# Performance work log

Measured on AMD Instinct MI355X. Metric: run time of the kernel, lower is better.

## Reference

```python
import jax, jax.numpy as jnp
import numpy as np

F32 = jnp.float32
FP8_MAX = 448.0          # E4M3 max normal
MIN_NORM_EXP = -6.0      # smallest normal exponent for E4M3 (bias 7)


def _floor_log2(a):
    """Exact floor(log2(a)) for a>0 (with correction for fp rounding); 0 -> 0."""
    a_safe = jnp.where(a > 0, a, 1.0)
    e = jnp.floor(jnp.log2(a_safe))
    p = jnp.exp2(e)
    e = jnp.where(a_safe >= 2.0 * p, e + 1.0, jnp.where(a_safe < p, e - 1.0, e))
    return jax.lax.stop_gradient(e)


def quant_e4m3(x):
    """Round-to-nearest-even quantization to FP8 E4M3 (saturating, no NaN)."""
    a = jnp.abs(x)
    e = jnp.maximum(_floor_log2(a), MIN_NORM_EXP)
    step = jnp.exp2(e - 3.0)                 # mantissa ULP (3 mantissa bits)
    q = jnp.round(a / step) * step           # jnp.round = round-half-even
    q = jnp.minimum(q, FP8_MAX)
    q = jnp.where(a > 0, q, 0.0)
    return jnp.where(x < 0, -q, q)


def bits_to_float(b):
    """Decode [..., 8] spike bits (sign, e3..e0, m2..m0) to float32 E4M3 value."""
    sign = 1.0 - 2.0 * b[..., 0]
    exp = b[..., 1] * 8.0 + b[..., 2] * 4.0 + b[..., 3] * 2.0 + b[..., 4]
    man = b[..., 5] * 4.0 + b[..., 6] * 2.0 + b[..., 7]
    mag = jnp.where(exp > 0,
                    (1.0 + man / 8.0) * jnp.exp2(exp - 7.0),   # normal
                    (man / 8.0) * jnp.exp2(MIN_NORM_EXP))       # subnormal
    return sign * mag


def float_to_bits(x):
    """Encode an FP8-representable float32 into [..., 8] spike bits."""
    sgn = (x < 0).astype(F32)
    a = jnp.abs(x)
    e = jnp.clip(_floor_log2(a), MIN_NORM_EXP, 8.0)
    is_norm = a >= jnp.exp2(MIN_NORM_EXP)
    ef = jnp.where(is_norm, e + 7.0, 0.0)
    man = jnp.where(is_norm, a * jnp.exp2(-e) * 8.0 - 8.0, a * jnp.exp2(9.0))
    man = jnp.clip(jnp.round(man), 0.0, 7.0)

    def bit(v, k):
        return jnp.floor(v / (2.0 ** k)) % 2.0

    return jnp.stack([sgn,
                      bit(ef, 3), bit(ef, 2), bit(ef, 1), bit(ef, 0),
                      bit(man, 2), bit(man, 1), bit(man, 0)], axis=-1)


B, IN, OUT = 256, 512, 1024


def setup_inputs() -> dict:
    key = jax.random.key(0)
    kx, kw = jax.random.split(key)
    # random floats -> quantize to FP8 -> encode as spike bits (valid pulses)
    x_f = jax.random.normal(kx, (B, IN), F32)
    w_f = jax.random.normal(kw, (OUT, IN), F32) * (1.0 / 32.0)  # keep accum < 448
    x = float_to_bits(quant_e4m3(x_f))                 # [B, IN, 8]
    weight_pulse = float_to_bits(quant_e4m3(w_f))      # [OUT, IN, 8]
    return {"x": x, "weight_pulse": weight_pulse}


def reference(x, weight_pulse):
    # SpikeFP8Linear_Fast, mode='sequential':
    # products[i] = fp8(x_i * w_i); acc = fp8(...fp8(p0 + p1) + ... + p_{N-1})
    xf = bits_to_float(x)             # [B, IN]
    wf = bits_to_float(weight_pulse)  # [OUT, IN]

    p0 = quant_e4m3(xf[:, 0][:, None] * wf[None, :, 0])  # [B, OUT]
    xs = jnp.moveaxis(xf[:, 1:], 1, 0)  # [IN-1, B]
    ws = jnp.moveaxis(wf[:, 1:], 1, 0)  # [IN-1, OUT]

    def step(acc, xw):
        xi, wi = xw
        p = quant_e4m3(xi[:, None] * wi[None, :])
        return quant_e4m3(acc + p), None

    acc, _ = jax.lax.scan(step, p0, (xs, ws))
    return float_to_bits(acc)  # [B, OUT, 8]
```

## Files before the change

### kernel.cpp

```cpp
#include <hip/hip_runtime.h>

#define B_DIM 256
#define IN_DIM 512
#define OUT_DIM 1024

typedef __attribute__((__ext_vector_type__(2))) float v2f;

__device__ __forceinline__ float dec_pair(float4 a, float4 b) {
    int ef  = ((int)a.y << 3) | ((int)a.z << 2) | ((int)a.w << 1) | (int)b.x;
    int man = ((int)b.y << 2) | ((int)b.z << 1) | (int)b.w;
    float mag;
    if (ef > 0)
        mag = __uint_as_float(((unsigned)(ef + 120) << 23) | ((unsigned)man << 20));
    else
        mag = (float)man * 0.001953125f;
    return (a.x != 0.0f) ? -mag : mag;
}

__global__ void k_decode(const float* __restrict__ xbits,
                         const float* __restrict__ wbits,
                         float* __restrict__ xf, float* __restrict__ wt) {
    int v = blockIdx.x * 256 + threadIdx.x;
    if (v < B_DIM * IN_DIM) {
        const float4* p = (const float4*)xbits + (size_t)v * 2;
        xf[v] = dec_pair(p[0], p[1]);
    } else {
        int u = v - B_DIM * IN_DIM;
        const float4* p = (const float4*)wbits + (size_t)u * 2;
        float val = dec_pair(p[0], p[1]);
        int o = u >> 9, i = u & 511;
        wt[((size_t)(i >> 2) * OUT_DIM + o) * 4 + (i & 3)] = val;
    }
}

__device__ __forceinline__ void store8(float* __restrict__ out, int idx, float v) {
    unsigned au = __float_as_uint(v) & 0x7fffffffu;
    float sgn = (v < 0.0f) ? 1.0f : 0.0f;
    int ef, man;
    if (au >= 0x3c800000u) {
        ef  = (int)(au >> 23) - 120;
        man = (int)((au >> 20) & 7u);
    } else {
        ef  = 0;
        man = (int)(__uint_as_float(au) * 512.0f);
    }
    float4 lo = make_float4(sgn,
                            (float)((ef >> 3) & 1), (float)((ef >> 2) & 1),
                            (float)((ef >> 1) & 1));
    float4 hi = make_float4((float)(ef & 1),
                            (float)((man >> 2) & 1), (float)((man >> 1) & 1),
                            (float)(man & 1));
    float4* op = (float4*)(out + (size_t)idx * 8);
    op[0] = lo;
    op[1] = hi;
}

__global__ __launch_bounds__(256) void k_main(const float* __restrict__ xf,
                                              const float* __restrict__ wt,
                                              float* __restrict__ out) {
    int tid  = threadIdx.x;
    int lane = tid & 63;
    int wid  = tid >> 6;
    int o  = blockIdx.x * 64 + lane;
    int b0 = __builtin_amdgcn_readfirstlane(blockIdx.y * 8 + wid * 2);

    const float* xa = xf + (size_t)b0 * IN_DIM;
    const float* xb = xa + IN_DIM;
    const float4* wq = (const float4*)wt + o;

    v2f acc = {0.0f, 0.0f};

    float4 wA[4], wB[4];
#pragma unroll
    for (int d = 0; d < 4; ++d) {
        wA[d] = wq[(size_t)(2 * d) * OUT_DIM];
        wB[d] = wq[(size_t)(2 * d + 1) * OUT_DIM];
    }
    float xav[2][8], xbv[2][8];
#pragma unroll
    for (int d = 0; d < 2; ++d)
#pragma unroll
        for (int k = 0; k < 8; ++k) {
            xav[d][k] = xa[d * 8 + k];
            xbv[d][k] = xb[d * 8 + k];
        }

    for (int go = 0; go < 64; go += 4) {
#pragma unroll
        for (int ph = 0; ph < 4; ++ph) {
            int g = go + ph;
            float4 cwA = wA[ph], cwB = wB[ph];
            wA[ph] = wq[(size_t)(2 * (g + 4)) * OUT_DIM];
            wB[ph] = wq[(size_t)(2 * (g + 4) + 1) * OUT_DIM];

            int xs = ph & 1;
            float wk[8] = {cwA.x, cwA.y, cwA.z, cwA.w,
                           cwB.x, cwB.y, cwB.z, cwB.w};
            v2f pf[8];
#pragma unroll
            for (int k = 0; k < 8; ++k) {
                v2f xp = {xav[xs][k], xbv[xs][k]};
                v2f wv = {wk[k], wk[k]};
                v2f p = xp * wv;
                int pq = __builtin_amdgcn_cvt_pk_fp8_f32(p.x, p.y, 0, false);
                pf[k] = __builtin_amdgcn_cvt_pk_f32_fp8(pq, false);
            }
            {
                const float* nxa = xa + (size_t)(g + 2) * 8;
                const float* nxb = xb + (size_t)(g + 2) * 8;
#pragma unroll
                for (int k = 0; k < 8; ++k) {
                    xav[xs][k] = nxa[k];
                    xbv[xs][k] = nxb[k];
                }
            }
#pragma unroll
            for (int k = 0; k < 8; ++k) {
                v2f s = acc + pf[k];
                int sq = __builtin_amdgcn_cvt_pk_fp8_f32(s.x, s.y, 0, false);
                acc = __builtin_amdgcn_cvt_pk_f32_fp8(sq, false);
            }
        }
    }

    store8(out, b0 * OUT_DIM + o, acc.x);
    store8(out, (b0 + 1) * OUT_DIM + o, acc.y);
}

extern "C" void kernel_launch(void* const* d_in, const int* in_sizes, int n_in,
                              void* d_out, int out_size, void* d_ws, size_t ws_size,
                              hipStream_t stream) {
    const float* xb = (const float*)d_in[0];
    const float* wb = (const float*)d_in[1];
    float* out = (float*)d_out;

    float* xf = (float*)d_ws;
    float* wt = (float*)d_ws + B_DIM * IN_DIM;

    int total = B_DIM * IN_DIM + OUT_DIM * IN_DIM;
    k_decode<<<dim3(total / 256), dim3(256), 0, stream>>>(xb, wb, xf, wt);

    dim3 grid(OUT_DIM / 64, B_DIM / 8);
    k_main<<<grid, dim3(256), 0, stream>>>(xf, wt, out);
}
```

Before: 99.60 us.

## Stage interleaved x rows in LDS and software-pipeline product computation

Each wave copies its two batch rows of decoded x into shared memory, interleaved so that one float4 read gives paired (xa, xb) values. The x reads in the loop come from LDS instead of scalar global loads. The products for the next group are computed ahead of the dependent quantized accumulation chain, so independent multiply/convert work can overlap the serial chain's latency. The grid axes are also swapped so consecutive blocks share the same weight columns, at the cost of extra registers and a __syncthreads.

Result: no change. 98.26 us (-1.3%).

```diff
diff --git a/kernel.cpp b/kernel.cpp
--- a/kernel.cpp
+++ b/kernel.cpp
@@ -55,18 +55,44 @@
     op[1] = hi;
 }
 
+__device__ __forceinline__ void products8(v2f* pf, const float4* xc,
+                                          float4 cwA, float4 cwB) {
+    float wk[8] = {cwA.x, cwA.y, cwA.z, cwA.w, cwB.x, cwB.y, cwB.z, cwB.w};
+    const v2f* xp = (const v2f*)xc;
+#pragma unroll
+    for (int k = 0; k < 8; ++k) {
+        v2f wv = {wk[k], wk[k]};
+        v2f p = xp[k] * wv;
+        int pq = __builtin_amdgcn_cvt_pk_fp8_f32(p.x, p.y, 0, false);
+        pf[k] = __builtin_amdgcn_cvt_pk_f32_fp8(pq, false);
+    }
+}
+
 __global__ __launch_bounds__(256) void k_main(const float* __restrict__ xf,
                                               const float* __restrict__ wt,
                                               float* __restrict__ out) {
+    __shared__ float xs[8 * IN_DIM + 32];
     int tid  = threadIdx.x;
     int lane = tid & 63;
     int wid  = tid >> 6;
-    int o  = blockIdx.x * 64 + lane;
-    int b0 = __builtin_amdgcn_readfirstlane(blockIdx.y * 8 + wid * 2);
+    int o  = blockIdx.y * 64 + lane;
+    int b0 = blockIdx.x * 8 + wid * 2;
 
-    const float* xa = xf + (size_t)b0 * IN_DIM;
-    const float* xb = xa + IN_DIM;
-    const float4* wq = (const float4*)wt + o;
+    {
+        const float4* ra = (const float4*)(xf + (size_t)b0 * IN_DIM) + lane * 2;
+        const float4* rb = (const float4*)(xf + (size_t)(b0 + 1) * IN_DIM) + lane * 2;
+        float4 a0 = ra[0], a1 = ra[1];
+        float4 c0 = rb[0], c1 = rb[1];
+        float4* dst = (float4*)(xs + (size_t)wid * 2 * IN_DIM) + lane * 4;
+        dst[0] = make_float4(a0.x, c0.x, a0.y, c0.y);
+        dst[1] = make_float4(a0.z, c0.z, a0.w, c0.w);
+        dst[2] = make_float4(a1.x, c1.x, a1.y, c1.y);
+        dst[3] = make_float4(a1.z, c1.z, a1.w, c1.w);
+    }
+    __syncthreads();
+
+    const float4* xls = (const float4*)(xs + (size_t)wid * 2 * IN_DIM);
+    const float4* wq  = (const float4*)wt + o;
 
     v2f acc = {0.0f, 0.0f};
 
@@ -76,43 +102,28 @@
         wA[d] = wq[(size_t)(2 * d) * OUT_DIM];
         wB[d] = wq[(size_t)(2 * d + 1) * OUT_DIM];
     }
-    float xav[2][8], xbv[2][8];
-#pragma unroll
-    for (int d = 0; d < 2; ++d)
-#pragma unroll
-        for (int k = 0; k < 8; ++k) {
-            xav[d][k] = xa[d * 8 + k];
-            xbv[d][k] = xb[d * 8 + k];
-        }
+    float4 xc0 = xls[0], xc1 = xls[1], xc2 = xls[2], xc3 = xls[3];
+    v2f pf[8];
+    {
+        float4 xc[4] = {xc0, xc1, xc2, xc3};
+        products8(pf, xc, wA[0], wB[0]);
+    }
+    xc0 = xls[4]; xc1 = xls[5]; xc2 = xls[6]; xc3 = xls[7];
 
     for (int go = 0; go < 64; go += 4) {
 #pragma unroll
         for (int ph = 0; ph < 4; ++ph) {
             int g = go + ph;
-            float4 cwA = wA[ph], cwB = wB[ph];
+            v2f pf_next[8];
+            {
+                float4 xc[4] = {xc0, xc1, xc2, xc3};
+                products8(pf_next, xc, wA[(ph + 1) & 3], wB[(ph + 1) & 3]);
+            }
             wA[ph] = wq[(size_t)(2 * (g + 4)) * OUT_DIM];
             wB[ph] = wq[(size_t)(2 * (g + 4) + 1) * OUT_DIM];
-
-            int xs = ph & 1;
-            float wk[8] = {cwA.x, cwA.y, cwA.z, cwA.w,
-                           cwB.x, cwB.y, cwB.z, cwB.w};
-            v2f pf[8];
-#pragma unroll
-            for (int k = 0; k < 8; ++k) {
-                v2f xp = {xav[xs][k], xbv[xs][k]};
-                v2f wv = {wk[k], wk[k]};
-                v2f p = xp * wv;
-                int pq = __builtin_amdgcn_cvt_pk_fp8_f32(p.x, p.y, 0, false);
-                pf[k] = __builtin_amdgcn_cvt_pk_f32_fp8(pq, false);
-            }
             {
-                const float* nxa = xa + (size_t)(g + 2) * 8;
-                const float* nxb = xb + (size_t)(g + 2) * 8;
-#pragma unroll
-                for (int k = 0; k < 8; ++k) {
-                    xav[xs][k] = nxa[k];
-                    xbv[xs][k] = nxb[k];
-                }
+                const float4* xn = xls + 4 * (g + 2);
+                xc0 = xn[0]; xc1 = xn[1]; xc2 = xn[2]; xc3 = xn[3];
             }
 #pragma unroll
             for (int k = 0; k < 8; ++k) {
@@ -120,6 +131,8 @@
                 int sq = __builtin_amdgcn_cvt_pk_fp8_f32(s.x, s.y, 0, false);
                 acc = __builtin_amdgcn_cvt_pk_f32_fp8(sq, false);
             }
+#pragma unroll
+            for (int k = 0; k < 8; ++k) pf[k] = pf_next[k];
         }
     }
 
@@ -140,6 +153,6 @@
     int total = B_DIM * IN_DIM + OUT_DIM * IN_DIM;
     k_decode<<<dim3(total / 256), dim3(256), 0, stream>>>(xb, wb, xf, wt);
 
-    dim3 grid(OUT_DIM / 64, B_DIM / 8);
+    dim3 grid(B_DIM / 8, OUT_DIM / 64);
     k_main<<<grid, dim3(256), 0, stream>>>(xf, wt, out);
 }
```

## Replace FP8 convert round-trips with float magic-number rounding and stage x in LDS

Applied to the files above, without the earlier changes.

Replaces the hardware fp8 pack/unpack round-trips for product and accumulator quantization with pure float arithmetic. Products are rounded by adding and subtracting an exponent-scaled magic constant, and the sum uses a Dekker-style split. Each thread now computes one batch row instead of a packed pair. The x rows are staged in shared memory and the grid is swapped so batch varies fastest. This aims to shorten the serial dependency chain per accumulate step, but drops the 2-wide packing and relies on the rounding tricks matching E4M3 saturation and subnormal behaviour.

New measurement: 109.0 us. +9.5%, slower.

```diff
diff --git a/kernel.cpp b/kernel.cpp
--- a/kernel.cpp
+++ b/kernel.cpp
@@ -3,8 +3,6 @@
 #define B_DIM 256
 #define IN_DIM 512
 #define OUT_DIM 1024
-
-typedef __attribute__((__ext_vector_type__(2))) float v2f;
 
 __device__ __forceinline__ float dec_pair(float4 a, float4 b) {
     int ef  = ((int)a.y << 3) | ((int)a.z << 2) | ((int)a.w << 1) | (int)b.x;
@@ -55,76 +53,88 @@
     op[1] = hi;
 }
 
+__device__ __forceinline__ float qprod(float x, float w) {
+#pragma clang fp contract(off)
+    float p  = x * w;
+    float E  = __uint_as_float(__float_as_uint(p) & 0x7f800000u);
+    float Ec = fmaxf(E, 0.015625f);
+    float M  = Ec * 1572864.0f;
+    float t  = p + M;
+    return t - M;
+}
+
+__device__ __forceinline__ float dek(float s) {
+#pragma clang fp contract(off)
+    float p1 = __builtin_fmaf(s, 1048576.0f, s);
+    float d  = p1 - s;
+    return p1 - d;
+}
+
 __global__ __launch_bounds__(256) void k_main(const float* __restrict__ xf,
                                               const float* __restrict__ wt,
                                               float* __restrict__ out) {
+    __shared__ float xs[4 * IN_DIM + 32];
     int tid  = threadIdx.x;
     int lane = tid & 63;
     int wid  = tid >> 6;
-    int o  = blockIdx.x * 64 + lane;
-    int b0 = __builtin_amdgcn_readfirstlane(blockIdx.y * 8 + wid * 2);
+    int o = blockIdx.y * 64 + lane;
+    int b = blockIdx.x * 4 + wid;
 
-    const float* xa = xf + (size_t)b0 * IN_DIM;
-    const float* xb = xa + IN_DIM;
-    const float4* wq = (const float4*)wt + o;
+    {
+        const float4* src = (const float4*)(xf + (size_t)blockIdx.x * 4 * IN_DIM);
+        float4* dst = (float4*)xs;
+        dst[tid]       = src[tid];
+        dst[tid + 256] = src[tid + 256];
+    }
+    __syncthreads();
 
-    v2f acc = {0.0f, 0.0f};
+    const float4* xls = (const float4*)(xs + (size_t)wid * IN_DIM);
+    const float4* wq  = (const float4*)wt + o;
+
+    float acc = 0.0f;
 
     float4 wA[4], wB[4];
+    {
+        const float4* wp = wq;
 #pragma unroll
-    for (int d = 0; d < 4; ++d) {
-        wA[d] = wq[(size_t)(2 * d) * OUT_DIM];
-        wB[d] = wq[(size_t)(2 * d + 1) * OUT_DIM];
+        for (int d = 0; d < 4; ++d) {
+            wA[d] = wp[0];
+            wB[d] = wp[OUT_DIM];
+            wp += 2 * OUT_DIM;
+        }
     }
-    float xav[2][8], xbv[2][8];
-#pragma unroll
-    for (int d = 0; d < 2; ++d)
-#pragma unroll
-        for (int k = 0; k < 8; ++k) {
-            xav[d][k] = xa[d * 8 + k];
-            xbv[d][k] = xb[d * 8 + k];
-        }
+    const float4* wqp = wq + (size_t)8 * OUT_DIM;
+
+    float4 xc0 = xls[0], xc1 = xls[1];
+    const float4* xlp = xls + 2;
 
     for (int go = 0; go < 64; go += 4) {
 #pragma unroll
         for (int ph = 0; ph < 4; ++ph) {
-            int g = go + ph;
+            float4 xn0 = xlp[0], xn1 = xlp[1];
+            xlp += 2;
             float4 cwA = wA[ph], cwB = wB[ph];
-            wA[ph] = wq[(size_t)(2 * (g + 4)) * OUT_DIM];
-            wB[ph] = wq[(size_t)(2 * (g + 4) + 1) * OUT_DIM];
+            wA[ph] = wqp[0];
+            wB[ph] = wqp[OUT_DIM];
+            wqp += 2 * OUT_DIM;
 
-            int xs = ph & 1;
             float wk[8] = {cwA.x, cwA.y, cwA.z, cwA.w,
                            cwB.x, cwB.y, cwB.z, cwB.w};
-            v2f pf[8];
+            float xk[8] = {xc0.x, xc0.y, xc0.z, xc0.w,
+                           xc1.x, xc1.y, xc1.z, xc1.w};
+            float pf[8];
 #pragma unroll
-            for (int k = 0; k < 8; ++k) {
-                v2f xp = {xav[xs][k], xbv[xs][k]};
-                v2f wv = {wk[k], wk[k]};
-                v2f p = xp * wv;
-                int pq = __builtin_amdgcn_cvt_pk_fp8_f32(p.x, p.y, 0, false);
-                pf[k] = __builtin_amdgcn_cvt_pk_f32_fp8(pq, false);
-            }
-            {
-                const float* nxa = xa + (size_t)(g + 2) * 8;
-                const float* nxb = xb + (size_t)(g + 2) * 8;
+            for (int k = 0; k < 8; ++k)
+                pf[k] = qprod(xk[k], wk[k]);
 #pragma unroll
-                for (int k = 0; k < 8; ++k) {
-                    xav[xs][k] = nxa[k];
-                    xbv[xs][k] = nxb[k];
-                }
-            }
-#pragma unroll
-            for (int k = 0; k < 8; ++k) {
-                v2f s = acc + pf[k];
-                int sq = __builtin_amdgcn_cvt_pk_fp8_f32(s.x, s.y, 0, false);
-                acc = __builtin_amdgcn_cvt_pk_f32_fp8(sq, false);
-            }
+            for (int k = 0; k < 8; ++k)
+                acc = dek(acc + pf[k]);
+
+            xc0 = xn0; xc1 = xn1;
         }
     }
 
-    store8(out, b0 * OUT_DIM + o, acc.x);
-    store8(out, (b0 + 1) * OUT_DIM + o, acc.y);
+    store8(out, b * OUT_DIM + o, acc);
 }
 
 extern "C" void kernel_launch(void* const* d_in, const int* in_sizes, int n_in,
@@ -140,6 +150,6 @@
     int total = B_DIM * IN_DIM + OUT_DIM * IN_DIM;
     k_decode<<<dim3(total / 256), dim3(256), 0, stream>>>(xb, wb, xf, wt);
 
-    dim3 grid(OUT_DIM / 64, B_DIM / 8);
+    dim3 grid(B_DIM / 4, OUT_DIM / 64);
     k_main<<<grid, dim3(256), 0, stream>>>(xf, wt, out);
 }
```
